# Optimization experiments

Hardware: AMD Instinct MI355X
Metric: run time of the kernel (lower is better)

Reference implementation:

```python
import jax, jax.numpy as jnp
import numpy as np

T, B, D = 256, 16, 512          # time, batch, intermediate_dim (GRU is seq-first)
HR = 256                         # router_dim
EXPERT_DIMS = [0, 128, 256, 512]
NUM_TASKS = 4
COST_EXP = 1.0
BN_EPS = 1e-5


def _gru(x, w_ih, w_hh, b_ih, b_hh):
    """PyTorch-semantics GRU over axis 0. x: (T, ..., D) -> (T, ..., H).
    Works batched (T,B,D) or unbatched (N,D) exactly like nn.GRU."""
    H = w_hh.shape[1]
    gi = x @ w_ih.T + b_ih            # (T, ..., 3H) input projections, done once
    h0 = jnp.zeros(x.shape[1:-1] + (H,), x.dtype)

    def step(h, gi_t):
        gh = h @ w_hh.T + b_hh
        i_r, i_z, i_n = jnp.split(gi_t, 3, axis=-1)
        h_r, h_z, h_n = jnp.split(gh, 3, axis=-1)
        r = jax.nn.sigmoid(i_r + h_r)
        z = jax.nn.sigmoid(i_z + h_z)
        n = jnp.tanh(i_n + r * h_n)
        h_new = (1.0 - z) * n + z * h
        return h_new, h_new

    _, ys = jax.lax.scan(step, h0, gi)
    return ys


def setup_inputs() -> dict:
    key = jax.random.key(0)
    ks = iter(jax.random.split(key, 64))

    def p(shape, fan_in):
        return (jax.random.normal(next(ks), shape, jnp.float32) / np.sqrt(fan_in)).astype(jnp.float32)

    inp = {
        'x': jax.random.normal(next(ks), (T, B, D), jnp.float32),
        'task_ids': jax.random.randint(next(ks), (T, B), 0, NUM_TASKS),
        # router params
        'router_w_ih': p((3 * HR, D), D),
        'router_w_hh': p((3 * HR, HR), HR),
        'router_b_ih': jnp.zeros((3 * HR,), jnp.float32),
        'router_b_hh': jnp.zeros((3 * HR,), jnp.float32),
        'router_out_w': p((len(EXPERT_DIMS), HR), HR),
        'router_out_b': jnp.zeros((len(EXPERT_DIMS),), jnp.float32),
    }
    for i, H in enumerate(EXPERT_DIMS):
        if H == 0:
            continue
        inp[f'e{i}_w_ih'] = p((3 * H, D), D)
        inp[f'e{i}_w_hh'] = p((3 * H, H), H)
        inp[f'e{i}_b_ih'] = jnp.zeros((3 * H,), jnp.float32)
        inp[f'e{i}_b_hh'] = jnp.zeros((3 * H,), jnp.float32)
        inp[f'e{i}_bn_g'] = jnp.ones((H,), jnp.float32)
        inp[f'e{i}_bn_b'] = jnp.zeros((H,), jnp.float32)
        inp[f'e{i}_out_w'] = p((D, H), H)
        inp[f'e{i}_out_b'] = jnp.zeros((D,), jnp.float32)
    return inp


def reference(x, task_ids,
              router_w_ih, router_w_hh, router_b_ih, router_b_hh,
              router_out_w, router_out_b,
              e1_w_ih, e1_w_hh, e1_b_ih, e1_b_hh, e1_bn_g, e1_bn_b, e1_out_w, e1_out_b,
              e2_w_ih, e2_w_hh, e2_b_ih, e2_b_hh, e2_bn_g, e2_bn_b, e2_out_w, e2_out_b,
              e3_w_ih, e3_w_hh, e3_b_ih, e3_b_hh, e3_bn_g, e3_bn_b, e3_out_w, e3_out_b):
    E = len(EXPERT_DIMS)
    # ---- router: GRU -> ReLU -> Linear -> softmax ----
    hs = _gru(x, router_w_ih, router_w_hh, router_b_ih, router_b_hh)   # (T,B,HR)
    logits = jax.nn.relu(hs) @ router_out_w.T + router_out_b           # (T,B,E)
    raw = jax.nn.softmax(logits, axis=-1)                              # raw_router_output
    # no dropout configured -> router_output == raw, all experts active

    # ---- task expert usage losses ----
    costs = jnp.asarray([d ** COST_EXP for d in EXPERT_DIMS], logits.dtype)
    eul = jnp.einsum('tbe,e->tb', raw, costs).reshape(-1)
    tflat = task_ids.reshape(-1)
    sums = jax.ops.segment_sum(eul, tflat, num_segments=NUM_TASKS)
    cnts = jax.ops.segment_sum(jnp.ones_like(eul), tflat, num_segments=NUM_TASKS)
    task_losses = sums / cnts                                           # (NUM_TASKS,)

    # ---- experts: each sees the flat (N,D) tokens as ONE unbatched GRU sequence ----
    flat_x = x.reshape(-1, D)                                           # (N,D)
    gates = raw.reshape(-1, E)                                          # (N,E)
    out = gates[:, 0:1] * flat_x                                        # expert 0 = identity

    eps = [(e1_w_ih, e1_w_hh, e1_b_ih, e1_b_hh, e1_bn_g, e1_bn_b, e1_out_w, e1_out_b),
           (e2_w_ih, e2_w_hh, e2_b_ih, e2_b_hh, e2_bn_g, e2_bn_b, e2_out_w, e2_out_b),
           (e3_w_ih, e3_w_hh, e3_b_ih, e3_b_hh, e3_bn_g, e3_bn_b, e3_out_w, e3_out_b)]
    for i, (w_ih, w_hh, b_ih, b_hh, g, b, ow, ob) in enumerate(eps, start=1):
        h = _gru(flat_x, w_ih, w_hh, b_ih, b_hh)                        # (N,H) unbatched seq
        mu = h.mean(0)
        var = ((h - mu) ** 2).mean(0)                                   # biased var (train-mode BN)
        hn = (h - mu) / jnp.sqrt(var + BN_EPS) * g + b
        eo = jax.nn.relu(hn) @ ow.T + ob                                # (N,D)
        out = out + gates[:, i:i + 1] * eo

    final_output = out.reshape(T, B, D)
    return final_output, raw, task_losses
```

## Files before the change

### kernel.cpp

```cpp
#include <hip/hip_runtime.h>
#include <math.h>

constexpr int TT = 256, BB = 16, DD = 512;
constexpr int NTOK = 4096;
constexpr int RTOT = 3456;
constexpr int E1OFF = 768, E2OFF = 1152, E3OFF = 1920;

constexpr size_t OFF_TSUM = 0;
constexpr size_t OFF_TCNT = 16;
constexpr size_t OFF_CNT  = 32;
constexpr size_t ZBYTES   = 64;
constexpr size_t OFF_GI   = 4096;
constexpr size_t OFF_HS   = OFF_GI  + (size_t)NTOK*RTOT*4;
constexpr size_t OFF_HA3  = OFF_HS  + (size_t)NTOK*256*4;
constexpr size_t OFF_HA2  = OFF_HA3 + (size_t)NTOK*512*4;
constexpr size_t OFF_HA1  = OFF_HA2 + (size_t)NTOK*256*4;
constexpr size_t OFF_AP   = OFF_HA1 + (size_t)NTOK*128*4;
constexpr size_t OFF_MU   = OFF_AP  + (size_t)NTOK*896*4;
constexpr size_t OFF_RSTD = OFF_MU  + 896*4;
constexpr size_t POISON_BYTES = (size_t)NTOK*(256+512+256+128)*4;

__device__ __forceinline__ bool is_poison(float v) {
  return __float_as_uint(v) == 0xAAAAAAAAu;
}

__global__ __launch_bounds__(256) void gemm1_kernel(
    const float* __restrict__ X,
    const float* __restrict__ wR, const float* __restrict__ w1,
    const float* __restrict__ w2, const float* __restrict__ w3,
    const float* __restrict__ bR, const float* __restrict__ b1,
    const float* __restrict__ b2, const float* __restrict__ b3,
    float* __restrict__ GI)
{
  __shared__ float At[32*64];
  __shared__ float Bt[32*64];
  const int n0 = blockIdx.x * 64;
  const int r0 = blockIdx.y * 64;
  const float* W; const float* bias; int rs;
  if (r0 < 768)       { W = wR; bias = bR; rs = 0; }
  else if (r0 < 1152) { W = w1; bias = b1; rs = 768; }
  else if (r0 < 1920) { W = w2; bias = b2; rs = 1152; }
  else                { W = w3; bias = b3; rs = 1920; }
  const int lr0 = r0 - rs;
  const int tid = threadIdx.x;
  const int lm = tid & 63, lk4 = tid >> 6;
  const int tx = tid & 15, ty = tid >> 4;
  float acc[4][4];
#pragma unroll
  for (int i = 0; i < 4; ++i)
#pragma unroll
    for (int q = 0; q < 4; ++q) acc[i][q] = 0.f;

  for (int kb = 0; kb < 512; kb += 32) {
    const float4 a0 = *(const float4*)(X + (size_t)(n0+lm)*512 + kb + lk4*8);
    const float4 a1 = *(const float4*)(X + (size_t)(n0+lm)*512 + kb + lk4*8 + 4);
    const float4 c0 = *(const float4*)(W + (size_t)(lr0+lm)*512 + kb + lk4*8);
    const float4 c1 = *(const float4*)(W + (size_t)(lr0+lm)*512 + kb + lk4*8 + 4);
    __syncthreads();
    At[(lk4*8+0)*64+lm]=a0.x; At[(lk4*8+1)*64+lm]=a0.y; At[(lk4*8+2)*64+lm]=a0.z; At[(lk4*8+3)*64+lm]=a0.w;
    At[(lk4*8+4)*64+lm]=a1.x; At[(lk4*8+5)*64+lm]=a1.y; At[(lk4*8+6)*64+lm]=a1.z; At[(lk4*8+7)*64+lm]=a1.w;
    Bt[(lk4*8+0)*64+lm]=c0.x; Bt[(lk4*8+1)*64+lm]=c0.y; Bt[(lk4*8+2)*64+lm]=c0.z; Bt[(lk4*8+3)*64+lm]=c0.w;
    Bt[(lk4*8+4)*64+lm]=c1.x; Bt[(lk4*8+5)*64+lm]=c1.y; Bt[(lk4*8+6)*64+lm]=c1.z; Bt[(lk4*8+7)*64+lm]=c1.w;
    __syncthreads();
#pragma unroll
    for (int k = 0; k < 32; ++k) {
      const float4 av = *(const float4*)&At[k*64 + ty*4];
      const float4 bv = *(const float4*)&Bt[k*64 + tx*4];
      acc[0][0]=fmaf(av.x,bv.x,acc[0][0]); acc[0][1]=fmaf(av.x,bv.y,acc[0][1]); acc[0][2]=fmaf(av.x,bv.z,acc[0][2]); acc[0][3]=fmaf(av.x,bv.w,acc[0][3]);
      acc[1][0]=fmaf(av.y,bv.x,acc[1][0]); acc[1][1]=fmaf(av.y,bv.y,acc[1][1]); acc[1][2]=fmaf(av.y,bv.z,acc[1][2]); acc[1][3]=fmaf(av.y,bv.w,acc[1][3]);
      acc[2][0]=fmaf(av.z,bv.x,acc[2][0]); acc[2][1]=fmaf(av.z,bv.y,acc[2][1]); acc[2][2]=fmaf(av.z,bv.z,acc[2][2]); acc[2][3]=fmaf(av.z,bv.w,acc[2][3]);
      acc[3][0]=fmaf(av.w,bv.x,acc[3][0]); acc[3][1]=fmaf(av.w,bv.y,acc[3][1]); acc[3][2]=fmaf(av.w,bv.z,acc[3][2]); acc[3][3]=fmaf(av.w,bv.w,acc[3][3]);
    }
  }
  const float4 bb = *(const float4*)(bias + lr0 + tx*4);
#pragma unroll
  for (int i = 0; i < 4; ++i) {
    float4 o;
    o.x = acc[i][0] + bb.x; o.y = acc[i][1] + bb.y; o.z = acc[i][2] + bb.z; o.w = acc[i][3] + bb.w;
    *(float4*)(GI + (size_t)(n0+ty*4+i)*RTOT + r0 + tx*4) = o;
  }
}

struct ScanArgs {
  const float* GI;
  const float* rwhh; const float* rbhh; float* hs;
  const float* w1; const float* b1; float* ha1;
  const float* w2; const float* b2; float* ha2;
  const float* w3; const float* b3; float* ha3;
  int* cnt;
};

template<int H, int OPW>
__device__ void expert_scan(const float* __restrict__ GIe, const float* __restrict__ whh,
                            const float* __restrict__ bhh, float* __restrict__ hall,
                            float* __restrict__ sm, int wg)
{
  constexpr int KCN = 512 / OPW;
  constexpr bool SINGLE = (OPW == H);
  const int tid = threadIdx.x;
  const int j = tid / KCN, kc = tid % KCN;
  const int jg = wg * OPW + j;

  float4 wr[8], wz[8], wn[8];
#pragma unroll
  for (int i4 = 0; i4 < 8; ++i4) {
    const int kk = kc * 32 + ((i4 + kc) & 7) * 4;
    wr[i4] = *(const float4*)(whh + (size_t)jg * H + kk);
    wz[i4] = *(const float4*)(whh + (size_t)(H + jg) * H + kk);
    wn[i4] = *(const float4*)(whh + (size_t)(2*H + jg) * H + kk);
  }
  float gbr = 0.f, gbz = 0.f, gbn = 0.f;
  float gr0 = 0.f, gz0 = 0.f, gn0 = 0.f, gr1 = 0.f, gz1 = 0.f, gn1 = 0.f;
  if (kc == 0) {
    gbr = bhh[jg]; gbz = bhh[H + jg]; gbn = bhh[2*H + jg];
    gr0 = GIe[jg]; gz0 = GIe[H + jg]; gn0 = GIe[2*H + jg];
    const float* g1 = GIe + RTOT;
    gr1 = g1[jg]; gz1 = g1[H + jg]; gn1 = g1[2*H + jg];
  }
  if (SINGLE) {
    if (tid < H) sm[tid] = 0.f;
    __syncthreads();
  }
  for (int t = 0; t < NTOK; ++t) {
    float gr2 = 0.f, gz2 = 0.f, gn2 = 0.f;
    if (kc == 0 && t + 2 < NTOK) {
      const float* g = GIe + (size_t)(t + 2) * RTOT;
      gr2 = g[jg]; gz2 = g[H + jg]; gn2 = g[2*H + jg];
    }
    const float* hbuf;
    if (SINGLE) {
      hbuf = sm + (size_t)(t & 1) * H;
    } else {
      float val = 0.f;
      if (tid < H && t > 0) {
        const volatile float* p = (const volatile float*)(hall + (size_t)(t - 1) * H + tid);
        val = *p;
        while (is_poison(val)) val = *p;
      }
      __syncthreads();
      if (tid < H) sm[tid] = val;
      __syncthreads();
      hbuf = sm;
    }
    float pr = 0.f, pz = 0.f, pn = 0.f;
#pragma unroll
    for (int i4 = 0; i4 < 8; ++i4) {
      const float4 h4 = *(const float4*)(hbuf + kc * 32 + ((i4 + kc) & 7) * 4);
      pr = fmaf(wr[i4].x, h4.x, pr); pr = fmaf(wr[i4].y, h4.y, pr);
      pr = fmaf(wr[i4].z, h4.z, pr); pr = fmaf(wr[i4].w, h4.w, pr);
      pz = fmaf(wz[i4].x, h4.x, pz); pz = fmaf(wz[i4].y, h4.y, pz);
      pz = fmaf(wz[i4].z, h4.z, pz); pz = fmaf(wz[i4].w, h4.w, pz);
      pn = fmaf(wn[i4].x, h4.x, pn); pn = fmaf(wn[i4].y, h4.y, pn);
      pn = fmaf(wn[i4].z, h4.z, pn); pn = fmaf(wn[i4].w, h4.w, pn);
    }
#pragma unroll
    for (int off = KCN / 2; off; off >>= 1) {
      pr += __shfl_down(pr, off); pz += __shfl_down(pz, off); pn += __shfl_down(pn, off);
    }
    if (kc == 0) {
      const float hprev = hbuf[jg];
      const float rg = 1.f / (1.f + expf(-(gr0 + gbr + pr)));
      const float zg = 1.f / (1.f + expf(-(gz0 + gbz + pz)));
      const float nn = tanhf(gn0 + rg * (pn + gbn));
      const float hn = (1.f - zg) * nn + zg * hprev;
      if (SINGLE) {
        sm[(size_t)((t + 1) & 1) * H + jg] = hn;
        hall[(size_t)t * H + jg] = hn;
      } else {
        *(volatile float*)(hall + (size_t)t * H + jg) = hn;
      }
    }
    if (SINGLE) __syncthreads();
    gr0 = gr1; gz0 = gz1; gn0 = gn1;
    gr1 = gr2; gz1 = gz2; gn1 = gn2;
  }
}

__device__ void router_scan(const float* __restrict__ GI, const float* __restrict__ whh,
                            const float* __restrict__ bhh, float* __restrict__ hs,
                            float* __restrict__ sm, int wg)
{
  float* hsmB = sm;
  float* pbuf = sm + 16 * 260;
  const int tid = threadIdx.x;
  const int j = tid >> 4, kc = tid & 15;
  const int jg = wg * 32 + j;
  float4 wr4[4], wz4[4], wn4[4];
#pragma unroll
  for (int i4 = 0; i4 < 4; ++i4) {
    const int kk = kc * 16 + ((i4 + kc) & 3) * 4;
    wr4[i4] = *(const float4*)(whh + (size_t)jg * 256 + kk);
    wz4[i4] = *(const float4*)(whh + (size_t)(256 + jg) * 256 + kk);
    wn4[i4] = *(const float4*)(whh + (size_t)(512 + jg) * 256 + kk);
  }
  const int b2 = tid >> 5, j2 = tid & 31;
  const int jg2 = wg * 32 + j2;
  const float gbr = bhh[jg2], gbz = bhh[256 + jg2], gbn = bhh[512 + jg2];
  float gr0, gz0, gn0, gr1, gz1, gn1;
  { const float* g = GI + (size_t)b2 * RTOT;        gr0 = g[jg2]; gz0 = g[256 + jg2]; gn0 = g[512 + jg2]; }
  { const float* g = GI + (size_t)(16 + b2) * RTOT; gr1 = g[jg2]; gz1 = g[256 + jg2]; gn1 = g[512 + jg2]; }
  const int pb = tid >> 5, pk = (tid & 31) * 8;

  for (int t = 0; t < TT; ++t) {
    float gr2 = 0.f, gz2 = 0.f, gn2 = 0.f;
    if (t + 2 < TT) {
      const float* g = GI + (size_t)((t + 2) * 16 + b2) * RTOT;
      gr2 = g[jg2]; gz2 = g[256 + jg2]; gn2 = g[512 + jg2];
    }
    float v[8];
    if (t == 0) {
#pragma unroll
      for (int u = 0; u < 8; ++u) v[u] = 0.f;
    } else {
      const volatile float* q = (const volatile float*)(hs + (size_t)(t - 1) * 4096 + tid * 8);
#pragma unroll
      for (int u = 0; u < 8; ++u) v[u] = q[u];
      bool bad = true;
      while (bad) {
        bad = false;
#pragma unroll
        for (int u = 0; u < 8; ++u)
          if (is_poison(v[u])) { v[u] = q[u]; bad = true; }
      }
    }
    __syncthreads();
    *(float4*)(hsmB + pb * 260 + pk)     = make_float4(v[0], v[1], v[2], v[3]);
    *(float4*)(hsmB + pb * 260 + pk + 4) = make_float4(v[4], v[5], v[6], v[7]);
    __syncthreads();
    float ar[16], az[16], an[16];
#pragma unroll
    for (int b = 0; b < 16; ++b) { ar[b] = 0.f; az[b] = 0.f; an[b] = 0.f; }
#pragma unroll
    for (int i4 = 0; i4 < 4; ++i4) {
      const int col = kc * 16 + ((i4 + kc) & 3) * 4;
#pragma unroll
      for (int b = 0; b < 16; ++b) {
        const float4 h4 = *(const float4*)(hsmB + b * 260 + col);
        ar[b] = fmaf(wr4[i4].x, h4.x, ar[b]); ar[b] = fmaf(wr4[i4].y, h4.y, ar[b]);
        ar[b] = fmaf(wr4[i4].z, h4.z, ar[b]); ar[b] = fmaf(wr4[i4].w, h4.w, ar[b]);
        az[b] = fmaf(wz4[i4].x, h4.x, az[b]); az[b] = fmaf(wz4[i4].y, h4.y, az[b]);
        az[b] = fmaf(wz4[i4].z, h4.z, az[b]); az[b] = fmaf(wz4[i4].w, h4.w, az[b]);
        an[b] = fmaf(wn4[i4].x, h4.x, an[b]); an[b] = fmaf(wn4[i4].y, h4.y, an[b]);
        an[b] = fmaf(wn4[i4].z, h4.z, an[b]); an[b] = fmaf(wn4[i4].w, h4.w, an[b]);
      }
    }
#pragma unroll
    for (int off = 8; off; off >>= 1) {
#pragma unroll
      for (int b = 0; b < 16; ++b) {
        ar[b] += __shfl_down(ar[b], off);
        az[b] += __shfl_down(az[b], off);
        an[b] += __shfl_down(an[b], off);
      }
    }
    if (kc == 0) {
#pragma unroll
      for (int b = 0; b < 16; ++b) {
        pbuf[(b * 32 + j) * 3 + 0] = ar[b];
        pbuf[(b * 32 + j) * 3 + 1] = az[b];
        pbuf[(b * 32 + j) * 3 + 2] = an[b];
      }
    }
    __syncthreads();
    const float pr = pbuf[(b2 * 32 + j2) * 3 + 0];
    const float pz = pbuf[(b2 * 32 + j2) * 3 + 1];
    const float pn = pbuf[(b2 * 32 + j2) * 3 + 2];
    const float hprev = hsmB[b2 * 260 + jg2];
    const float rg = 1.f / (1.f + expf(-(gr0 + gbr + pr)));
    const float zg = 1.f / (1.f + expf(-(gz0 + gbz + pz)));
    const float nn = tanhf(gn0 + rg * (pn + gbn));
    const float hn = (1.f - zg) * nn + zg * hprev;
    *(volatile float*)(hs + (size_t)t * 4096 + b2 * 256 + jg2) = hn;
    gr0 = gr1; gz0 = gz1; gn0 = gn1;
    gr1 = gr2; gz1 = gz2; gn1 = gn2;
  }
}

__global__ __launch_bounds__(512, 1) void scan_kernel(ScanArgs A)
{
  __shared__ float sm[16 * 260 + 1536];
  __shared__ int role_s[2];
  if (threadIdx.x == 0) {
    unsigned x;
    asm volatile("s_getreg_b32 %0, hwreg(HW_REG_XCC_ID)" : "=s"(x));
    const int xcd = (int)(x & 7u);
    role_s[0] = xcd;
    role_s[1] = atomicAdd(A.cnt + xcd, 1);
  }
  __syncthreads();
  const int xcd = role_s[0], r = role_s[1];
  if (xcd == 0)      { if (r < 16) expert_scan<512, 32>(A.GI + E3OFF, A.w3, A.b3, A.ha3, sm, r); }
  else if (xcd == 1) { if (r < 8)  router_scan(A.GI, A.rwhh, A.rbhh, A.hs, sm, r); }
  else if (xcd == 2) { if (r < 4)  expert_scan<256, 64>(A.GI + E2OFF, A.w2, A.b2, A.ha2, sm, r); }
  else if (xcd == 3) { if (r < 1)  expert_scan<128,128>(A.GI + E1OFF, A.w1, A.b1, A.ha1, sm, r); }
}

__global__ __launch_bounds__(256) void router_out_kernel(
    const float* __restrict__ hs, const float* __restrict__ ow, const float* __restrict__ ob,
    const int* __restrict__ tids, float* __restrict__ raw_out,
    float* __restrict__ tsum, float* __restrict__ tcnt)
{
  const int tid = threadIdx.x;
  const int lane = tid & 63, w = tid >> 6;
  const int n = blockIdx.x * 4 + w;
  float s0 = 0.f, s1 = 0.f, s2 = 0.f, s3 = 0.f;
#pragma unroll
  for (int q = 0; q < 4; ++q) {
    const int jj = lane + q * 64;
    float h = hs[(size_t)n * 256 + jj];
    h = h > 0.f ? h : 0.f;
    s0 = fmaf(h, ow[jj], s0);
    s1 = fmaf(h, ow[256 + jj], s1);
    s2 = fmaf(h, ow[512 + jj], s2);
    s3 = fmaf(h, ow[768 + jj], s3);
  }
  for (int off = 32; off; off >>= 1) {
    s0 += __shfl_xor(s0, off); s1 += __shfl_xor(s1, off);
    s2 += __shfl_xor(s2, off); s3 += __shfl_xor(s3, off);
  }
  if (lane == 0) {
    const float l0 = s0 + ob[0], l1 = s1 + ob[1], l2 = s2 + ob[2], l3 = s3 + ob[3];
    const float m = fmaxf(fmaxf(l0, l1), fmaxf(l2, l3));
    const float e0 = expf(l0 - m), e1 = expf(l1 - m), e2 = expf(l2 - m), e3 = expf(l3 - m);
    const float inv = 1.f / (e0 + e1 + e2 + e3);
    float4 rv; rv.x = e0 * inv; rv.y = e1 * inv; rv.z = e2 * inv; rv.w = e3 * inv;
    *(float4*)(raw_out + (size_t)n * 4) = rv;
    const float eul = rv.y * 128.f + rv.z * 256.f + rv.w * 512.f;
    const int tk = tids[n];
    atomicAdd(&tsum[tk], eul);
    atomicAdd(&tcnt[tk], 1.f);
  }
}

__global__ __launch_bounds__(256) void bn_stats_kernel(
    const float* __restrict__ h1, const float* __restrict__ h2, const float* __restrict__ h3,
    float* __restrict__ mu, float* __restrict__ rstd)
{
  const int c = blockIdx.x;
  const float* hp; int He, hc;
  if (c < 128)      { hp = h1; He = 128; hc = c; }
  else if (c < 384) { hp = h2; He = 256; hc = c - 128; }
  else              { hp = h3; He = 512; hc = c - 384; }
  float s = 0.f, s2 = 0.f;
  for (int r = threadIdx.x; r < NTOK; r += 256) {
    const float v = hp[(size_t)r * He + hc];
    s += v; s2 = fmaf(v, v, s2);
  }
  for (int off = 32; off; off >>= 1) { s += __shfl_xor(s, off); s2 += __shfl_xor(s2, off); }
  __shared__ float red[8];
  const int lane = threadIdx.x & 63, w = threadIdx.x >> 6;
  if (lane == 0) { red[w] = s; red[4 + w] = s2; }
  __syncthreads();
  if (threadIdx.x == 0) {
    const float S = red[0] + red[1] + red[2] + red[3];
    const float S2 = red[4] + red[5] + red[6] + red[7];
    const float m = S * (1.f / 4096.f);
    float v = S2 * (1.f / 4096.f) - m * m;
    v = v > 0.f ? v : 0.f;
    mu[c] = m;
    rstd[c] = 1.f / sqrtf(v + 1e-5f);
  }
}

__global__ __launch_bounds__(256) void aprime_kernel(
    const float* __restrict__ h1, const float* __restrict__ h2, const float* __restrict__ h3,
    const float* __restrict__ g1, const float* __restrict__ be1,
    const float* __restrict__ g2, const float* __restrict__ be2,
    const float* __restrict__ g3, const float* __restrict__ be3,
    const float* __restrict__ mu, const float* __restrict__ rstd,
    const float* __restrict__ raw, float* __restrict__ Ap,
    const float* __restrict__ tsum, const float* __restrict__ tcnt, float* __restrict__ tl_out)
{
  if (blockIdx.x == 4096) {
    if (threadIdx.x < 4) tl_out[threadIdx.x] = tsum[threadIdx.x] / tcnt[threadIdx.x];
    return;
  }
  const int n = blockIdx.x;
  for (int c = threadIdx.x; c < 896; c += 256) {
    const float* hp; const float* gg; const float* bb; int He, hc, e;
    if (c < 128)      { hp = h1; gg = g1; bb = be1; He = 128; hc = c;       e = 1; }
    else if (c < 384) { hp = h2; gg = g2; bb = be2; He = 256; hc = c - 128; e = 2; }
    else              { hp = h3; gg = g3; bb = be3; He = 512; hc = c - 384; e = 3; }
    const float h = hp[(size_t)n * He + hc];
    float v = (h - mu[c]) * rstd[c] * gg[hc] + bb[hc];
    v = v > 0.f ? v : 0.f;
    Ap[(size_t)n * 896 + c] = raw[(size_t)n * 4 + e] * v;
  }
}

__global__ __launch_bounds__(256) void out_gemm_kernel(
    const float* __restrict__ Ap,
    const float* __restrict__ ow1, const float* __restrict__ ow2, const float* __restrict__ ow3,
    const float* __restrict__ ob1, const float* __restrict__ ob2, const float* __restrict__ ob3,
    const float* __restrict__ X, const float* __restrict__ raw, float* __restrict__ out)
{
  __shared__ float At[32*64];
  __shared__ float Bt[32*64];
  const int n0 = blockIdx.x * 64;
  const int d0 = blockIdx.y * 64;
  const int tid = threadIdx.x;
  const int lm = tid & 63, lk4 = tid >> 6;
  const int tx = tid & 15, ty = tid >> 4;
  float acc[4][4];
#pragma unroll
  for (int i = 0; i < 4; ++i)
#pragma unroll
    for (int q = 0; q < 4; ++q) acc[i][q] = 0.f;

  for (int kb = 0; kb < 896; kb += 32) {
    const float* W; int He, ko;
    if (kb < 128)      { W = ow1; He = 128; ko = 0; }
    else if (kb < 384) { W = ow2; He = 256; ko = 128; }
    else               { W = ow3; He = 512; ko = 384; }
    const float4 a0 = *(const float4*)(Ap + (size_t)(n0+lm)*896 + kb + lk4*8);
    const float4 a1 = *(const float4*)(Ap + (size_t)(n0+lm)*896 + kb + lk4*8 + 4);
    const float4 c0 = *(const float4*)(W + (size_t)(d0+lm)*He + (kb - ko) + lk4*8);
    const float4 c1 = *(const float4*)(W + (size_t)(d0+lm)*He + (kb - ko) + lk4*8 + 4);
    __syncthreads();
    At[(lk4*8+0)*64+lm]=a0.x; At[(lk4*8+1)*64+lm]=a0.y; At[(lk4*8+2)*64+lm]=a0.z; At[(lk4*8+3)*64+lm]=a0.w;
    At[(lk4*8+4)*64+lm]=a1.x; At[(lk4*8+5)*64+lm]=a1.y; At[(lk4*8+6)*64+lm]=a1.z; At[(lk4*8+7)*64+lm]=a1.w;
    Bt[(lk4*8+0)*64+lm]=c0.x; Bt[(lk4*8+1)*64+lm]=c0.y; Bt[(lk4*8+2)*64+lm]=c0.z; Bt[(lk4*8+3)*64+lm]=c0.w;
    Bt[(lk4*8+4)*64+lm]=c1.x; Bt[(lk4*8+5)*64+lm]=c1.y; Bt[(lk4*8+6)*64+lm]=c1.z; Bt[(lk4*8+7)*64+lm]=c1.w;
    __syncthreads();
#pragma unroll
    for (int k = 0; k < 32; ++k) {
      const float4 av = *(const float4*)&At[k*64 + ty*4];
      const float4 bv = *(const float4*)&Bt[k*64 + tx*4];
      acc[0][0]=fmaf(av.x,bv.x,acc[0][0]); acc[0][1]=fmaf(av.x,bv.y,acc[0][1]); acc[0][2]=fmaf(av.x,bv.z,acc[0][2]); acc[0][3]=fmaf(av.x,bv.w,acc[0][3]);
      acc[1][0]=fmaf(av.y,bv.x,acc[1][0]); acc[1][1]=fmaf(av.y,bv.y,acc[1][1]); acc[1][2]=fmaf(av.y,bv.z,acc[1][2]); acc[1][3]=fmaf(av.y,bv.w,acc[1][3]);
      acc[2][0]=fmaf(av.z,bv.x,acc[2][0]); acc[2][1]=fmaf(av.z,bv.y,acc[2][1]); acc[2][2]=fmaf(av.z,bv.z,acc[2][2]); acc[2][3]=fmaf(av.z,bv.w,acc[2][3]);
      acc[3][0]=fmaf(av.w,bv.x,acc[3][0]); acc[3][1]=fmaf(av.w,bv.y,acc[3][1]); acc[3][2]=fmaf(av.w,bv.z,acc[3][2]); acc[3][3]=fmaf(av.w,bv.w,acc[3][3]);
    }
  }
#pragma unroll
  for (int i = 0; i < 4; ++i) {
    const int n = n0 + ty * 4 + i;
    const float4 g  = *(const float4*)(raw + (size_t)n * 4);
    const float4 xv = *(const float4*)(X + (size_t)n * 512 + d0 + tx * 4);
    const float4 o1 = *(const float4*)(ob1 + d0 + tx * 4);
    const float4 o2 = *(const float4*)(ob2 + d0 + tx * 4);
    const float4 o3 = *(const float4*)(ob3 + d0 + tx * 4);
    float4 o;
    o.x = acc[i][0] + g.x*xv.x + g.y*o1.x + g.z*o2.x + g.w*o3.x;
    o.y = acc[i][1] + g.x*xv.y + g.y*o1.y + g.z*o2.y + g.w*o3.y;
    o.z = acc[i][2] + g.x*xv.z + g.y*o1.z + g.z*o2.z + g.w*o3.z;
    o.w = acc[i][3] + g.x*xv.w + g.y*o1.w + g.z*o2.w + g.w*o3.w;
    *(float4*)(out + (size_t)n * 512 + d0 + tx * 4) = o;
  }
}

extern "C" void kernel_launch(void* const* d_in, const int* in_sizes, int n_in,
                              void* d_out, int out_size, void* d_ws, size_t ws_size,
                              hipStream_t stream) {
  const float* x    = (const float*)d_in[0];
  const int*   tids = (const int*)d_in[1];
  const float* rwih = (const float*)d_in[2];
  const float* rwhh = (const float*)d_in[3];
  const float* rbih = (const float*)d_in[4];
  const float* rbhh = (const float*)d_in[5];
  const float* row  = (const float*)d_in[6];
  const float* rob  = (const float*)d_in[7];
  const float* w1ih = (const float*)d_in[8];
  const float* w1hh = (const float*)d_in[9];
  const float* b1ih = (const float*)d_in[10];
  const float* b1hh = (const float*)d_in[11];
  const float* bn1g = (const float*)d_in[12];
  const float* bn1b = (const float*)d_in[13];
  const float* ow1  = (const float*)d_in[14];
  const float* ob1  = (const float*)d_in[15];
  const float* w2ih = (const float*)d_in[16];
  const float* w2hh = (const float*)d_in[17];
  const float* b2ih = (const float*)d_in[18];
  const float* b2hh = (const float*)d_in[19];
  const float* bn2g = (const float*)d_in[20];
  const float* bn2b = (const float*)d_in[21];
  const float* ow2  = (const float*)d_in[22];
  const float* ob2  = (const float*)d_in[23];
  const float* w3ih = (const float*)d_in[24];
  const float* w3hh = (const float*)d_in[25];
  const float* b3ih = (const float*)d_in[26];
  const float* b3hh = (const float*)d_in[27];
  const float* bn3g = (const float*)d_in[28];
  const float* bn3b = (const float*)d_in[29];
  const float* ow3  = (const float*)d_in[30];
  const float* ob3  = (const float*)d_in[31];

  char* ws = (char*)d_ws;
  float* tsum = (float*)(ws + OFF_TSUM);
  float* tcnt = (float*)(ws + OFF_TCNT);
  int*   cnt  = (int*)(ws + OFF_CNT);
  float* GI   = (float*)(ws + OFF_GI);
  float* hs   = (float*)(ws + OFF_HS);
  float* ha3  = (float*)(ws + OFF_HA3);
  float* ha2  = (float*)(ws + OFF_HA2);
  float* ha1  = (float*)(ws + OFF_HA1);
  float* Ap   = (float*)(ws + OFF_AP);
  float* mu   = (float*)(ws + OFF_MU);
  float* rstd = (float*)(ws + OFF_RSTD);

  float* outp = (float*)d_out;
  float* rawp = outp + (size_t)NTOK * DD;
  float* tlp  = rawp + (size_t)NTOK * 4;

  hipMemsetAsync(ws, 0, ZBYTES, stream);
  hipMemsetAsync(ws + OFF_HS, 0xAA, POISON_BYTES, stream);

  gemm1_kernel<<<dim3(64, 54), 256, 0, stream>>>(x, rwih, w1ih, w2ih, w3ih,
                                                 rbih, b1ih, b2ih, b3ih, GI);

  ScanArgs sa;
  sa.GI = GI; sa.rwhh = rwhh; sa.rbhh = rbhh; sa.hs = hs;
  sa.w1 = w1hh; sa.b1 = b1hh; sa.ha1 = ha1;
  sa.w2 = w2hh; sa.b2 = b2hh; sa.ha2 = ha2;
  sa.w3 = w3hh; sa.b3 = b3hh; sa.ha3 = ha3;
  sa.cnt = cnt;
  scan_kernel<<<dim3(320), dim3(512), 0, stream>>>(sa);

  router_out_kernel<<<dim3(1024), 256, 0, stream>>>(hs, row, rob, tids, rawp, tsum, tcnt);
  bn_stats_kernel<<<dim3(896), 256, 0, stream>>>(ha1, ha2, ha3, mu, rstd);
  aprime_kernel<<<dim3(4097), 256, 0, stream>>>(ha1, ha2, ha3, bn1g, bn1b, bn2g, bn2b,
                                                bn3g, bn3b, mu, rstd, rawp, Ap,
                                                tsum, tcnt, tlp);

  out_gemm_kernel<<<dim3(64, 8), 256, 0, stream>>>(Ap, ow1, ow2, ow3, ob1, ob2, ob3,
                                                   x, rawp, outp);
}
```

Before: 6.761 ms.

## Add producer wavefront and LDS flags to replace block barriers in expert scans

The scan kernel grows from 512 to 576 threads, giving each block one extra wavefront. In the multi-block expert scans, that wavefront polls global memory for the previous hidden state, writes it into a double-buffered LDS slot and raises an LDS flag. The compute wavefronts spin on the flag instead of running two __syncthreads per step. The single-block expert replaces its per-step barrier with per-wave LDS progress flags that readers poll for the minimum. The router scan is adapted so the extra wavefront stays idle but still joins the barriers. The aim is to cut barrier overhead on the sequential critical path, at the cost of busy-wait spinning and fragile memory-ordering assumptions.

```diff
diff --git a/kernel.cpp b/kernel.cpp
--- a/kernel.cpp
+++ b/kernel.cpp
@@ -91,16 +91,53 @@
 };
 
 template<int H, int OPW>
-__device__ void expert_scan(const float* __restrict__ GIe, const float* __restrict__ whh,
-                            const float* __restrict__ bhh, float* __restrict__ hall,
-                            float* __restrict__ sm, int wg)
+__device__ void expert_scan2(const float* __restrict__ GIe, const float* __restrict__ whh,
+                             const float* __restrict__ bhh, float* __restrict__ hall,
+                             float* sm, int wg)
 {
   constexpr int KCN = 512 / OPW;
-  constexpr bool SINGLE = (OPW == H);
+  float* buf = sm;
+  volatile int* flag = (volatile int*)(sm + 2*H);
   const int tid = threadIdx.x;
+
+  for (int i = tid; i < 2*H; i += 576) buf[i] = 0.f;
+  if (tid == 0) *flag = 0;
+  __syncthreads();
+
+  if (tid >= 512) {
+    const int l = tid - 512;
+    for (int t = 1; t < NTOK; ++t) {
+      const volatile float* src = (const volatile float*)(hall + (size_t)(t-1)*H);
+      float v0 = src[l*4+0], v1 = src[l*4+1], v2 = src[l*4+2], v3 = src[l*4+3];
+      float u0 = 0.f, u1 = 0.f, u2 = 0.f, u3 = 0.f;
+      if constexpr (H > 256) {
+        u0 = src[256+l*4+0]; u1 = src[256+l*4+1]; u2 = src[256+l*4+2]; u3 = src[256+l*4+3];
+      }
+      for (;;) {
+        bool bad = false;
+        if (is_poison(v0)) { v0 = src[l*4+0]; bad = true; }
+        if (is_poison(v1)) { v1 = src[l*4+1]; bad = true; }
+        if (is_poison(v2)) { v2 = src[l*4+2]; bad = true; }
+        if (is_poison(v3)) { v3 = src[l*4+3]; bad = true; }
+        if constexpr (H > 256) {
+          if (is_poison(u0)) { u0 = src[256+l*4+0]; bad = true; }
+          if (is_poison(u1)) { u1 = src[256+l*4+1]; bad = true; }
+          if (is_poison(u2)) { u2 = src[256+l*4+2]; bad = true; }
+          if (is_poison(u3)) { u3 = src[256+l*4+3]; bad = true; }
+        }
+        if (!bad) break;
+      }
+      float* dst = buf + (size_t)(t & 1) * H;
+      *(float4*)(dst + l*4) = make_float4(v0, v1, v2, v3);
+      if constexpr (H > 256) *(float4*)(dst + 256 + l*4) = make_float4(u0, u1, u2, u3);
+      asm volatile("s_waitcnt lgkmcnt(0)" ::: "memory");
+      if (l == 0) *flag = t;
+    }
+    return;
+  }
+
   const int j = tid / KCN, kc = tid % KCN;
   const int jg = wg * OPW + j;
-
   float4 wr[8], wz[8], wn[8];
 #pragma unroll
   for (int i4 = 0; i4 < 8; ++i4) {
@@ -117,31 +154,18 @@
     const float* g1 = GIe + RTOT;
     gr1 = g1[jg]; gz1 = g1[H + jg]; gn1 = g1[2*H + jg];
   }
-  if (SINGLE) {
-    if (tid < H) sm[tid] = 0.f;
-    __syncthreads();
-  }
   for (int t = 0; t < NTOK; ++t) {
     float gr2 = 0.f, gz2 = 0.f, gn2 = 0.f;
     if (kc == 0 && t + 2 < NTOK) {
       const float* g = GIe + (size_t)(t + 2) * RTOT;
       gr2 = g[jg]; gz2 = g[H + jg]; gn2 = g[2*H + jg];
     }
-    const float* hbuf;
-    if (SINGLE) {
-      hbuf = sm + (size_t)(t & 1) * H;
-    } else {
-      float val = 0.f;
-      if (tid < H && t > 0) {
-        const volatile float* p = (const volatile float*)(hall + (size_t)(t - 1) * H + tid);
-        val = *p;
-        while (is_poison(val)) val = *p;
-      }
-      __syncthreads();
-      if (tid < H) sm[tid] = val;
-      __syncthreads();
-      hbuf = sm;
-    }
+    if (t > 0) {
+      while (*flag < t) {}
+    }
+    asm volatile("" ::: "memory");
+    __builtin_amdgcn_sched_barrier(0);
+    const float* hbuf = buf + (size_t)(t & 1) * H;
     float pr = 0.f, pz = 0.f, pn = 0.f;
 #pragma unroll
     for (int i4 = 0; i4 < 8; ++i4) {
@@ -163,120 +187,208 @@
       const float zg = 1.f / (1.f + expf(-(gz0 + gbz + pz)));
       const float nn = tanhf(gn0 + rg * (pn + gbn));
       const float hn = (1.f - zg) * nn + zg * hprev;
-      if (SINGLE) {
-        sm[(size_t)((t + 1) & 1) * H + jg] = hn;
-        hall[(size_t)t * H + jg] = hn;
-      } else {
-        *(volatile float*)(hall + (size_t)t * H + jg) = hn;
-      }
-    }
-    if (SINGLE) __syncthreads();
+      *(volatile float*)(hall + (size_t)t * H + jg) = hn;
+    }
     gr0 = gr1; gz0 = gz1; gn0 = gn1;
     gr1 = gr2; gz1 = gz2; gn1 = gn2;
   }
 }
 
+template<int H, int OPW>
+__device__ void expert_scan_single(const float* __restrict__ GIe, const float* __restrict__ whh,
+                                   const float* __restrict__ bhh, float* __restrict__ hall,
+                                   float* sm, int )
+{
+  constexpr int KCN = 512 / OPW;
+  float* buf = sm;
+  volatile int* wflag = (volatile int*)(sm + 2*H);
+  const int tid = threadIdx.x;
+  for (int i = tid; i < 2*H; i += 576) buf[i] = 0.f;
+  if (tid < 8) wflag[tid] = 0;
+  __syncthreads();
+  if (tid >= 512) return;
+
+  const int w = tid >> 6;
+  const int j = tid / KCN, kc = tid % KCN;
+  float4 wr[8], wz[8], wn[8];
+#pragma unroll
+  for (int i4 = 0; i4 < 8; ++i4) {
+    const int kk = kc * 32 + ((i4 + kc) & 7) * 4;
+    wr[i4] = *(const float4*)(whh + (size_t)j * H + kk);
+    wz[i4] = *(const float4*)(whh + (size_t)(H + j) * H + kk);
+    wn[i4] = *(const float4*)(whh + (size_t)(2*H + j) * H + kk);
+  }
+  float gbr = 0.f, gbz = 0.f, gbn = 0.f;
+  float gr0 = 0.f, gz0 = 0.f, gn0 = 0.f, gr1 = 0.f, gz1 = 0.f, gn1 = 0.f;
+  if (kc == 0) {
+    gbr = bhh[j]; gbz = bhh[H + j]; gbn = bhh[2*H + j];
+    gr0 = GIe[j]; gz0 = GIe[H + j]; gn0 = GIe[2*H + j];
+    const float* g1 = GIe + RTOT;
+    gr1 = g1[j]; gz1 = g1[H + j]; gn1 = g1[2*H + j];
+  }
+  for (int t = 0; t < NTOK; ++t) {
+    float gr2 = 0.f, gz2 = 0.f, gn2 = 0.f;
+    if (kc == 0 && t + 2 < NTOK) {
+      const float* g = GIe + (size_t)(t + 2) * RTOT;
+      gr2 = g[j]; gz2 = g[H + j]; gn2 = g[2*H + j];
+    }
+    if (t > 0) {
+      for (;;) {
+        int m0 = wflag[0], m1 = wflag[1], m2 = wflag[2], m3 = wflag[3];
+        int m4 = wflag[4], m5 = wflag[5], m6 = wflag[6], m7 = wflag[7];
+        int m = min(min(min(m0, m1), min(m2, m3)), min(min(m4, m5), min(m6, m7)));
+        if (m >= t) break;
+      }
+    }
+    asm volatile("" ::: "memory");
+    __builtin_amdgcn_sched_barrier(0);
+    const float* hbuf = buf + (size_t)(t & 1) * H;
+    float pr = 0.f, pz = 0.f, pn = 0.f;
+#pragma unroll
+    for (int i4 = 0; i4 < 8; ++i4) {
+      const float4 h4 = *(const float4*)(hbuf + kc * 32 + ((i4 + kc) & 7) * 4);
+      pr = fmaf(wr[i4].x, h4.x, pr); pr = fmaf(wr[i4].y, h4.y, pr);
+      pr = fmaf(wr[i4].z, h4.z, pr); pr = fmaf(wr[i4].w, h4.w, pr);
+      pz = fmaf(wz[i4].x, h4.x, pz); pz = fmaf(wz[i4].y, h4.y, pz);
+      pz = fmaf(wz[i4].z, h4.z, pz); pz = fmaf(wz[i4].w, h4.w, pz);
+      pn = fmaf(wn[i4].x, h4.x, pn); pn = fmaf(wn[i4].y, h4.y, pn);
+      pn = fmaf(wn[i4].z, h4.z, pn); pn = fmaf(wn[i4].w, h4.w, pn);
+    }
+#pragma unroll
+    for (int off = KCN / 2; off; off >>= 1) {
+      pr += __shfl_down(pr, off); pz += __shfl_down(pz, off); pn += __shfl_down(pn, off);
+    }
+    if (kc == 0) {
+      const float hprev = hbuf[j];
+      const float rg = 1.f / (1.f + expf(-(gr0 + gbr + pr)));
+      const float zg = 1.f / (1.f + expf(-(gz0 + gbz + pz)));
+      const float nn = tanhf(gn0 + rg * (pn + gbn));
+      const float hn = (1.f - zg) * nn + zg * hprev;
+      buf[(size_t)((t + 1) & 1) * H + j] = hn;
+      hall[(size_t)t * H + j] = hn;
+    }
+    asm volatile("s_waitcnt lgkmcnt(0)" ::: "memory");
+    if ((tid & 63) == 0) wflag[w] = t + 1;
+    gr0 = gr1; gz0 = gz1; gn0 = gn1;
+    gr1 = gr2; gz1 = gz2; gn1 = gn2;
+  }
+}
+
 __device__ void router_scan(const float* __restrict__ GI, const float* __restrict__ whh,
                             const float* __restrict__ bhh, float* __restrict__ hs,
-                            float* __restrict__ sm, int wg)
+                            float* sm, int wg)
 {
   float* hsmB = sm;
   float* pbuf = sm + 16 * 260;
   const int tid = threadIdx.x;
-  const int j = tid >> 4, kc = tid & 15;
+  const bool act = (tid < 512);
+  const int j = (tid >> 4) & 31, kc = tid & 15;
   const int jg = wg * 32 + j;
   float4 wr4[4], wz4[4], wn4[4];
-#pragma unroll
-  for (int i4 = 0; i4 < 4; ++i4) {
-    const int kk = kc * 16 + ((i4 + kc) & 3) * 4;
-    wr4[i4] = *(const float4*)(whh + (size_t)jg * 256 + kk);
-    wz4[i4] = *(const float4*)(whh + (size_t)(256 + jg) * 256 + kk);
-    wn4[i4] = *(const float4*)(whh + (size_t)(512 + jg) * 256 + kk);
-  }
-  const int b2 = tid >> 5, j2 = tid & 31;
+  if (act) {
+#pragma unroll
+    for (int i4 = 0; i4 < 4; ++i4) {
+      const int kk = kc * 16 + ((i4 + kc) & 3) * 4;
+      wr4[i4] = *(const float4*)(whh + (size_t)jg * 256 + kk);
+      wz4[i4] = *(const float4*)(whh + (size_t)(256 + jg) * 256 + kk);
+      wn4[i4] = *(const float4*)(whh + (size_t)(512 + jg) * 256 + kk);
+    }
+  }
+  const int b2 = (tid >> 5) & 15, j2 = tid & 31;
   const int jg2 = wg * 32 + j2;
-  const float gbr = bhh[jg2], gbz = bhh[256 + jg2], gbn = bhh[512 + jg2];
-  float gr0, gz0, gn0, gr1, gz1, gn1;
-  { const float* g = GI + (size_t)b2 * RTOT;        gr0 = g[jg2]; gz0 = g[256 + jg2]; gn0 = g[512 + jg2]; }
-  { const float* g = GI + (size_t)(16 + b2) * RTOT; gr1 = g[jg2]; gz1 = g[256 + jg2]; gn1 = g[512 + jg2]; }
-  const int pb = tid >> 5, pk = (tid & 31) * 8;
+  float gbr = 0.f, gbz = 0.f, gbn = 0.f;
+  float gr0 = 0.f, gz0 = 0.f, gn0 = 0.f, gr1 = 0.f, gz1 = 0.f, gn1 = 0.f;
+  if (act) {
+    gbr = bhh[jg2]; gbz = bhh[256 + jg2]; gbn = bhh[512 + jg2];
+    { const float* g = GI + (size_t)b2 * RTOT;        gr0 = g[jg2]; gz0 = g[256 + jg2]; gn0 = g[512 + jg2]; }
+    { const float* g = GI + (size_t)(16 + b2) * RTOT; gr1 = g[jg2]; gz1 = g[256 + jg2]; gn1 = g[512 + jg2]; }
+  }
+  const int pb = (tid >> 5) & 15, pk = (tid & 31) * 8;
 
   for (int t = 0; t < TT; ++t) {
+    float v[8];
+    if (act) {
+      if (t == 0) {
+#pragma unroll
+        for (int u = 0; u < 8; ++u) v[u] = 0.f;
+      } else {
+        const volatile float* q = (const volatile float*)(hs + (size_t)(t - 1) * 4096 + tid * 8);
+#pragma unroll
+        for (int u = 0; u < 8; ++u) v[u] = q[u];
+        bool bad = true;
+        while (bad) {
+          bad = false;
+#pragma unroll
+          for (int u = 0; u < 8; ++u)
+            if (is_poison(v[u])) { v[u] = q[u]; bad = true; }
+        }
+      }
+    }
     float gr2 = 0.f, gz2 = 0.f, gn2 = 0.f;
-    if (t + 2 < TT) {
+    if (act && t + 2 < TT) {
       const float* g = GI + (size_t)((t + 2) * 16 + b2) * RTOT;
       gr2 = g[jg2]; gz2 = g[256 + jg2]; gn2 = g[512 + jg2];
     }
-    float v[8];
-    if (t == 0) {
-#pragma unroll
-      for (int u = 0; u < 8; ++u) v[u] = 0.f;
-    } else {
-      const volatile float* q = (const volatile float*)(hs + (size_t)(t - 1) * 4096 + tid * 8);
-#pragma unroll
-      for (int u = 0; u < 8; ++u) v[u] = q[u];
-      bool bad = true;
-      while (bad) {
-        bad = false;
-#pragma unroll
-        for (int u = 0; u < 8; ++u)
-          if (is_poison(v[u])) { v[u] = q[u]; bad = true; }
+    __syncthreads();
+    if (act) {
+      *(float4*)(hsmB + pb * 260 + pk)     = make_float4(v[0], v[1], v[2], v[3]);
+      *(float4*)(hsmB + pb * 260 + pk + 4) = make_float4(v[4], v[5], v[6], v[7]);
+    }
+    __syncthreads();
+    if (act) {
+      float ar[16], az[16], an[16];
+#pragma unroll
+      for (int b = 0; b < 16; ++b) { ar[b] = 0.f; az[b] = 0.f; an[b] = 0.f; }
+#pragma unroll
+      for (int i4 = 0; i4 < 4; ++i4) {
+        const int col = kc * 16 + ((i4 + kc) & 3) * 4;
+#pragma unroll
+        for (int b = 0; b < 16; ++b) {
+          const float4 h4 = *(const float4*)(hsmB + b * 260 + col);
+          ar[b] = fmaf(wr4[i4].x, h4.x, ar[b]); ar[b] = fmaf(wr4[i4].y, h4.y, ar[b]);
+          ar[b] = fmaf(wr4[i4].z, h4.z, ar[b]); ar[b] = fmaf(wr4[i4].w, h4.w, ar[b]);
+          az[b] = fmaf(wz4[i4].x, h4.x, az[b]); az[b] = fmaf(wz4[i4].y, h4.y, az[b]);
+          az[b] = fmaf(wz4[i4].z, h4.z, az[b]); az[b] = fmaf(wz4[i4].w, h4.w, az[b]);
+          an[b] = fmaf(wn4[i4].x, h4.x, an[b]); an[b] = fmaf(wn4[i4].y, h4.y, an[b]);
+          an[b] = fmaf(wn4[i4].z, h4.z, an[b]); an[b] = fmaf(wn4[i4].w, h4.w, an[b]);
+        }
       }
+#pragma unroll
+      for (int off = 8; off; off >>= 1) {
+#pragma unroll
+        for (int b = 0; b < 16; ++b) {
+          ar[b] += __shfl_down(ar[b], off);
+          az[b] += __shfl_down(az[b], off);
+          an[b] += __shfl_down(an[b], off);
+        }
+      }
+      if (kc == 0) {
+#pragma unroll
+        for (int b = 0; b < 16; ++b) {
+          pbuf[(b * 32 + j) * 3 + 0] = ar[b];
+          pbuf[(b * 32 + j) * 3 + 1] = az[b];
+          pbuf[(b * 32 + j) * 3 + 2] = an[b];
+        }
+      }
     }
     __syncthreads();
-    *(float4*)(hsmB + pb * 260 + pk)     = make_float4(v[0], v[1], v[2], v[3]);
-    *(float4*)(hsmB + pb * 260 + pk + 4) = make_float4(v[4], v[5], v[6], v[7]);
-    __syncthreads();
-    float ar[16], az[16], an[16];
-#pragma unroll
-    for (int b = 0; b < 16; ++b) { ar[b] = 0.f; az[b] = 0.f; an[b] = 0.f; }
-#pragma unroll
-    for (int i4 = 0; i4 < 4; ++i4) {
-      const int col = kc * 16 + ((i4 + kc) & 3) * 4;
-#pragma unroll
-      for (int b = 0; b < 16; ++b) {
-        const float4 h4 = *(const float4*)(hsmB + b * 260 + col);
-        ar[b] = fmaf(wr4[i4].x, h4.x, ar[b]); ar[b] = fmaf(wr4[i4].y, h4.y, ar[b]);
-        ar[b] = fmaf(wr4[i4].z, h4.z, ar[b]); ar[b] = fmaf(wr4[i4].w, h4.w, ar[b]);
-        az[b] = fmaf(wz4[i4].x, h4.x, az[b]); az[b] = fmaf(wz4[i4].y, h4.y, az[b]);
-        az[b] = fmaf(wz4[i4].z, h4.z, az[b]); az[b] = fmaf(wz4[i4].w, h4.w, az[b]);
-        an[b] = fmaf(wn4[i4].x, h4.x, an[b]); an[b] = fmaf(wn4[i4].y, h4.y, an[b]);
-        an[b] = fmaf(wn4[i4].z, h4.z, an[b]); an[b] = fmaf(wn4[i4].w, h4.w, an[b]);
-      }
-    }
-#pragma unroll
-    for (int off = 8; off; off >>= 1) {
-#pragma unroll
-      for (int b = 0; b < 16; ++b) {
-        ar[b] += __shfl_down(ar[b], off);
-        az[b] += __shfl_down(az[b], off);
-        an[b] += __shfl_down(an[b], off);
-      }
-    }
-    if (kc == 0) {
-#pragma unroll
-      for (int b = 0; b < 16; ++b) {
-        pbuf[(b * 32 + j) * 3 + 0] = ar[b];
-        pbuf[(b * 32 + j) * 3 + 1] = az[b];
-        pbuf[(b * 32 + j) * 3 + 2] = an[b];
-      }
-    }
-    __syncthreads();
-    const float pr = pbuf[(b2 * 32 + j2) * 3 + 0];
-    const float pz = pbuf[(b2 * 32 + j2) * 3 + 1];
-    const float pn = pbuf[(b2 * 32 + j2) * 3 + 2];
-    const float hprev = hsmB[b2 * 260 + jg2];
-    const float rg = 1.f / (1.f + expf(-(gr0 + gbr + pr)));
-    const float zg = 1.f / (1.f + expf(-(gz0 + gbz + pz)));
-    const float nn = tanhf(gn0 + rg * (pn + gbn));
-    const float hn = (1.f - zg) * nn + zg * hprev;
-    *(volatile float*)(hs + (size_t)t * 4096 + b2 * 256 + jg2) = hn;
-    gr0 = gr1; gz0 = gz1; gn0 = gn1;
-    gr1 = gr2; gz1 = gz2; gn1 = gn2;
-  }
-}
-
-__global__ __launch_bounds__(512, 1) void scan_kernel(ScanArgs A)
+    if (act) {
+      const float pr = pbuf[(b2 * 32 + j2) * 3 + 0];
+      const float pz = pbuf[(b2 * 32 + j2) * 3 + 1];
+      const float pn = pbuf[(b2 * 32 + j2) * 3 + 2];
+      const float hprev = hsmB[b2 * 260 + jg2];
+      const float rg = 1.f / (1.f + expf(-(gr0 + gbr + pr)));
+      const float zg = 1.f / (1.f + expf(-(gz0 + gbz + pz)));
+      const float nn = tanhf(gn0 + rg * (pn + gbn));
+      const float hn = (1.f - zg) * nn + zg * hprev;
+      *(volatile float*)(hs + (size_t)t * 4096 + b2 * 256 + jg2) = hn;
+      gr0 = gr1; gz0 = gz1; gn0 = gn1;
+      gr1 = gr2; gz1 = gz2; gn1 = gn2;
+    }
+  }
+}
+
+__global__ __launch_bounds__(576, 1) void scan_kernel(ScanArgs A)
 {
   __shared__ float sm[16 * 260 + 1536];
   __shared__ int role_s[2];
@@ -289,10 +401,10 @@
   }
   __syncthreads();
   const int xcd = role_s[0], r = role_s[1];
-  if (xcd == 0)      { if (r < 16) expert_scan<512, 32>(A.GI + E3OFF, A.w3, A.b3, A.ha3, sm, r); }
+  if (xcd == 0)      { if (r < 16) expert_scan2<512, 32>(A.GI + E3OFF, A.w3, A.b3, A.ha3, sm, r); }
   else if (xcd == 1) { if (r < 8)  router_scan(A.GI, A.rwhh, A.rbhh, A.hs, sm, r); }
-  else if (xcd == 2) { if (r < 4)  expert_scan<256, 64>(A.GI + E2OFF, A.w2, A.b2, A.ha2, sm, r); }
-  else if (xcd == 3) { if (r < 1)  expert_scan<128,128>(A.GI + E1OFF, A.w1, A.b1, A.ha1, sm, r); }
+  else if (xcd == 2) { if (r < 4)  expert_scan2<256, 64>(A.GI + E2OFF, A.w2, A.b2, A.ha2, sm, r); }
+  else if (xcd == 3) { if (r < 1)  expert_scan_single<128, 128>(A.GI + E1OFF, A.w1, A.b1, A.ha1, sm, r); }
 }
 
 __global__ __launch_bounds__(256) void router_out_kernel(
@@ -514,7 +626,7 @@
   sa.w2 = w2hh; sa.b2 = b2hh; sa.ha2 = ha2;
   sa.w3 = w3hh; sa.b3 = b3hh; sa.ha3 = ha3;
   sa.cnt = cnt;
-  scan_kernel<<<dim3(320), dim3(512), 0, stream>>>(sa);
+  scan_kernel<<<dim3(320), dim3(576), 0, stream>>>(sa);
 
   router_out_kernel<<<dim3(1024), 256, 0, stream>>>(hs, row, rob, tids, rawp, tsum, tcnt);
   bn_stats_kernel<<<dim3(896), 256, 0, stream>>>(ha1, ha2, ha3, mu, rstd);
```

Result: slower. 12.96 ms (+91.6%).

## Spread expert GRU scans across more workgroups with generic chunked hidden reduction

Applied to the files above, without the earlier changes.

Generalizes the expert recurrent scan so each thread covers a variable-size chunk of the hidden dimension, and launches more workgroups per expert (32/16/4 instead of 16/4/1) with fewer outputs each. The single-workgroup shared-memory path for the smallest expert is removed, so every expert now exchanges hidden state through global memory with poison-polling. This cuts per-step FMA work per workgroup but increases cross-workgroup synchronization traffic and global polling latency each timestep. A trivial FMA reorder in the router is also included.

```diff
diff --git a/kernel.cpp b/kernel.cpp
--- a/kernel.cpp
+++ b/kernel.cpp
@@ -96,15 +96,16 @@
                             float* __restrict__ sm, int wg)
 {
   constexpr int KCN = 512 / OPW;
-  constexpr bool SINGLE = (OPW == H);
+  constexpr int CHUNK = H / KCN;
+  constexpr int NF4 = CHUNK / 4;
   const int tid = threadIdx.x;
   const int j = tid / KCN, kc = tid % KCN;
   const int jg = wg * OPW + j;
 
-  float4 wr[8], wz[8], wn[8];
-#pragma unroll
-  for (int i4 = 0; i4 < 8; ++i4) {
-    const int kk = kc * 32 + ((i4 + kc) & 7) * 4;
+  float4 wr[NF4], wz[NF4], wn[NF4];
+#pragma unroll
+  for (int i4 = 0; i4 < NF4; ++i4) {
+    const int kk = kc * CHUNK + ((i4 + kc) & (NF4 - 1)) * 4;
     wr[i4] = *(const float4*)(whh + (size_t)jg * H + kk);
     wz[i4] = *(const float4*)(whh + (size_t)(H + jg) * H + kk);
     wn[i4] = *(const float4*)(whh + (size_t)(2*H + jg) * H + kk);
@@ -117,35 +118,25 @@
     const float* g1 = GIe + RTOT;
     gr1 = g1[jg]; gz1 = g1[H + jg]; gn1 = g1[2*H + jg];
   }
-  if (SINGLE) {
-    if (tid < H) sm[tid] = 0.f;
-    __syncthreads();
-  }
   for (int t = 0; t < NTOK; ++t) {
+    float val = 0.f;
+    if (tid < H && t > 0) {
+      const volatile float* p = (const volatile float*)(hall + (size_t)(t - 1) * H + tid);
+      val = *p;
+      while (is_poison(val)) val = *p;
+    }
+    __syncthreads();
+    if (tid < H) sm[tid] = val;
+    __syncthreads();
     float gr2 = 0.f, gz2 = 0.f, gn2 = 0.f;
     if (kc == 0 && t + 2 < NTOK) {
       const float* g = GIe + (size_t)(t + 2) * RTOT;
       gr2 = g[jg]; gz2 = g[H + jg]; gn2 = g[2*H + jg];
     }
-    const float* hbuf;
-    if (SINGLE) {
-      hbuf = sm + (size_t)(t & 1) * H;
-    } else {
-      float val = 0.f;
-      if (tid < H && t > 0) {
-        const volatile float* p = (const volatile float*)(hall + (size_t)(t - 1) * H + tid);
-        val = *p;
-        while (is_poison(val)) val = *p;
-      }
-      __syncthreads();
-      if (tid < H) sm[tid] = val;
-      __syncthreads();
-      hbuf = sm;
-    }
     float pr = 0.f, pz = 0.f, pn = 0.f;
 #pragma unroll
-    for (int i4 = 0; i4 < 8; ++i4) {
-      const float4 h4 = *(const float4*)(hbuf + kc * 32 + ((i4 + kc) & 7) * 4);
+    for (int i4 = 0; i4 < NF4; ++i4) {
+      const float4 h4 = *(const float4*)(sm + kc * CHUNK + ((i4 + kc) & (NF4 - 1)) * 4);
       pr = fmaf(wr[i4].x, h4.x, pr); pr = fmaf(wr[i4].y, h4.y, pr);
       pr = fmaf(wr[i4].z, h4.z, pr); pr = fmaf(wr[i4].w, h4.w, pr);
       pz = fmaf(wz[i4].x, h4.x, pz); pz = fmaf(wz[i4].y, h4.y, pz);
@@ -158,19 +149,13 @@
       pr += __shfl_down(pr, off); pz += __shfl_down(pz, off); pn += __shfl_down(pn, off);
     }
     if (kc == 0) {
-      const float hprev = hbuf[jg];
+      const float hprev = sm[jg];
       const float rg = 1.f / (1.f + expf(-(gr0 + gbr + pr)));
       const float zg = 1.f / (1.f + expf(-(gz0 + gbz + pz)));
       const float nn = tanhf(gn0 + rg * (pn + gbn));
       const float hn = (1.f - zg) * nn + zg * hprev;
-      if (SINGLE) {
-        sm[(size_t)((t + 1) & 1) * H + jg] = hn;
-        hall[(size_t)t * H + jg] = hn;
-      } else {
-        *(volatile float*)(hall + (size_t)t * H + jg) = hn;
-      }
-    }
-    if (SINGLE) __syncthreads();
+      *(volatile float*)(hall + (size_t)t * H + jg) = hn;
+    }
     gr0 = gr1; gz0 = gz1; gn0 = gn1;
     gr1 = gr2; gz1 = gz2; gn1 = gn2;
   }
@@ -241,7 +226,7 @@
         az[b] = fmaf(wz4[i4].x, h4.x, az[b]); az[b] = fmaf(wz4[i4].y, h4.y, az[b]);
         az[b] = fmaf(wz4[i4].z, h4.z, az[b]); az[b] = fmaf(wz4[i4].w, h4.w, az[b]);
         an[b] = fmaf(wn4[i4].x, h4.x, an[b]); an[b] = fmaf(wn4[i4].y, h4.y, an[b]);
-        an[b] = fmaf(wn4[i4].z, h4.z, an[b]); an[b] = fmaf(wn4[i4].w, h4.w, an[b]);
+        an[b] = fmaf(wn4[i4].w, h4.w, an[b]); an[b] = fmaf(wn4[i4].z, h4.z, an[b]);
       }
     }
 #pragma unroll
@@ -289,10 +274,10 @@
   }
   __syncthreads();
   const int xcd = role_s[0], r = role_s[1];
-  if (xcd == 0)      { if (r < 16) expert_scan<512, 32>(A.GI + E3OFF, A.w3, A.b3, A.ha3, sm, r); }
+  if (xcd == 0)      { if (r < 32) expert_scan<512, 16>(A.GI + E3OFF, A.w3, A.b3, A.ha3, sm, r); }
   else if (xcd == 1) { if (r < 8)  router_scan(A.GI, A.rwhh, A.rbhh, A.hs, sm, r); }
-  else if (xcd == 2) { if (r < 4)  expert_scan<256, 64>(A.GI + E2OFF, A.w2, A.b2, A.ha2, sm, r); }
-  else if (xcd == 3) { if (r < 1)  expert_scan<128,128>(A.GI + E1OFF, A.w1, A.b1, A.ha1, sm, r); }
+  else if (xcd == 2) { if (r < 16) expert_scan<256, 16>(A.GI + E2OFF, A.w2, A.b2, A.ha2, sm, r); }
+  else if (xcd == 3) { if (r < 4)  expert_scan<128, 32>(A.GI + E1OFF, A.w1, A.b1, A.ha1, sm, r); }
 }
 
 __global__ __launch_bounds__(256) void router_out_kernel(
```

Result: slower. 7.303 ms (+8.0%).
